# Performance work log

Measured on AMD Instinct MI355X. Metric: run time of the kernel, lower is better.

Reference implementation:

```python
import jax, jax.numpy as jnp
import numpy as np

N_NODES = 20000
N_EDGES = 160000
D_IN = 512
D_OUT = 64


def _propagate(x, src, dst, num_nodes):
    # SLPropagate with add_self_loops=False, normalize=False:
    # out[dst] += x[src]  (plain sum aggregation over incoming edges)
    return jax.ops.segment_sum(x[src], dst, num_segments=num_nodes)


def setup_inputs() -> dict:
    key = jax.random.key(0)
    k1, k2, k3, k4 = jax.random.split(key, 4)
    x = jax.random.normal(k1, (N_NODES, D_IN), dtype=jnp.float32)
    edge_index = jax.random.randint(k2, (2, N_EDGES), 0, N_NODES, dtype=jnp.int64)
    # torch.nn.Linear default init scale ~ 1/sqrt(fan_in)
    s = 1.0 / np.sqrt(D_IN)
    W1 = jax.random.uniform(k3, (D_IN, D_IN), dtype=jnp.float32, minval=-s, maxval=s)
    W2 = jax.random.uniform(k4, (D_OUT, D_IN), dtype=jnp.float32, minval=-s, maxval=s)
    return {"x": x, "edge_index": edge_index, "W1": W1, "W2": W2}


def reference(x, edge_index, W1, W2):
    num_nodes = x.shape[0]
    src, dst = edge_index[0], edge_index[1]
    h = _propagate(x, src, dst, num_nodes)          # [N, D_IN]
    h = jax.nn.relu(jnp.einsum('nd,ed->ne', h, W1))  # lin1 (no bias) + relu
    h = _propagate(h, src, dst, num_nodes)          # [N, D_IN]
    h = jnp.einsum('nd,od->no', h, W2)              # lin2 (no bias) -> [N, D_OUT]
    return jax.nn.log_softmax(h, axis=1)
```

## Files before the change

kernel.cpp:

```cpp
#include <hip/hip_runtime.h>

#define D 512
#define DOUT 64
#define MAXDEG 64

typedef __bf16 bf16x8 __attribute__((ext_vector_type(8)));
typedef float floatx4 __attribute__((ext_vector_type(4)));

__device__ __forceinline__ void async_cp16(const void* g, void* lds) {
    __builtin_amdgcn_global_load_lds(
        (__attribute__((address_space(1))) void*)(void*)g,
        (__attribute__((address_space(3))) void*)lds, 16, 0, 0);
}

__global__ __launch_bounds__(256) void prep_kernel(
        int* __restrict__ cnt, int nN, int zeroBlocks,
        __bf16* __restrict__ tzero,
        const float* __restrict__ W1, __bf16* __restrict__ w1b, int w1N8,
        const float* __restrict__ W2, __bf16* __restrict__ w2b, int w2N8) {
    int b = blockIdx.x;
    if (b < zeroBlocks) {
        int i4 = b * 1024 + threadIdx.x * 4;
        if (i4 + 3 < nN) *(int4*)(cnt + i4) = make_int4(0, 0, 0, 0);
        else {
            if (i4 + 0 < nN) cnt[i4 + 0] = 0;
            if (i4 + 1 < nN) cnt[i4 + 1] = 0;
            if (i4 + 2 < nN) cnt[i4 + 2] = 0;
        }
        return;
    }
    b -= zeroBlocks;
    if (b == 0) {
        ((unsigned*)tzero)[threadIdx.x] = 0u;
        return;
    }
    b -= 1;
    int w1Blocks = (w1N8 + 255) >> 8;
    const float* in; __bf16* outp; int n8;
    if (b < w1Blocks) { in = W1; outp = w1b; n8 = w1N8; }
    else { b -= w1Blocks; in = W2; outp = w2b; n8 = w2N8; }
    int i = b * 256 + threadIdx.x;
    if (i < n8) {
        const float4* p = (const float4*)in + (size_t)i * 2;
        float4 v0 = p[0], v1 = p[1];
        bf16x8 o;
        o[0] = (__bf16)v0.x; o[1] = (__bf16)v0.y; o[2] = (__bf16)v0.z; o[3] = (__bf16)v0.w;
        o[4] = (__bf16)v1.x; o[5] = (__bf16)v1.y; o[6] = (__bf16)v1.z; o[7] = (__bf16)v1.w;
        *((bf16x8*)outp + i) = o;
    }
}

__global__ __launch_bounds__(256, 3) void gemm1_fill(
        const float* __restrict__ Af, const __bf16* __restrict__ B,
        __bf16* __restrict__ Cout, int M, int gemmBlocks,
        const int* __restrict__ src, const int* __restrict__ dst,
        int* __restrict__ cnt, unsigned short* __restrict__ col, int nE) {
    if (blockIdx.x >= gemmBlocks) {
        int base = (blockIdx.x - gemmBlocks) * 256 + threadIdx.x;
        int stride = (gridDim.x - gemmBlocks) * 256;
        for (int e = base; e < nE; e += stride) {
            int d = dst[e];
            int slot = atomicAdd(&cnt[d], 1);
            if (slot < MAXDEG) col[(size_t)d * MAXDEG + slot] = (unsigned short)src[e];
        }
        return;
    }
    constexpr int BM = 128, BN = 128;
    __shared__ float  Asf[BM * 16 * 4];
    __shared__ __bf16 Bs[8 * BN * 8];

    const int qch = gemmBlocks >> 3, rch = gemmBlocks & 7;
    const int xcd = blockIdx.x & 7, jj = blockIdx.x >> 3;
    const int L = (xcd < rch ? xcd * (qch + 1) : rch * (qch + 1) + (xcd - rch) * qch) + jj;

    const int tid = threadIdx.x;
    const int w = tid >> 6, lane = tid & 63;
    const int wrow = w >> 1, wcol = w & 1;
    const int m0 = (L >> 2) * BM, n0 = (L & 3) * BN;
    const int quad = lane >> 4, l15 = lane & 15;

    const int srow = lane >> 3;
    const int skq  = (lane & 7) ^ (srow & 7);

    floatx4 acc[4][4] = {};

    for (int k0 = 0; k0 < D; k0 += 64) {
        #pragma unroll
        for (int c = 0; c < 8; ++c) {
            int P0 = (w * 8 + c) * 64;
            int P = P0 + lane;
            int rloc = P >> 4, cu = P & 15;
            int gr = m0 + rloc; if (gr > M - 1) gr = M - 1;
            async_cp16(Af + (size_t)gr * D + k0 + ((cu ^ (rloc & 15)) << 2),
                       &Asf[(size_t)P0 * 4]);
        }
        #pragma unroll
        for (int c = 0; c < 4; ++c) {
            int P0 = (w * 4 + c) * 64;
            int nn = n0 + (P0 >> 3) + srow;
            async_cp16(B + (size_t)nn * D + k0 + skq * 8, &Bs[(size_t)P0 * 8]);
        }
        __syncthreads();

        #pragma unroll
        for (int ksub = 0; ksub < 2; ++ksub) {
            const int kk = ksub * 4 + quad;
            bf16x8 af[4], bfr[4];
            #pragma unroll
            for (int mi = 0; mi < 4; ++mi) {
                int rr = wrow * 64 + mi * 16 + l15;
                int u0 = ((kk << 1)    ) ^ (rr & 15);
                int u1 = ((kk << 1) | 1) ^ (rr & 15);
                float4 f0 = *(const float4*)&Asf[(size_t)(rr * 16 + u0) * 4];
                float4 f1 = *(const float4*)&Asf[(size_t)(rr * 16 + u1) * 4];
                bf16x8 a_;
                a_[0] = (__bf16)f0.x; a_[1] = (__bf16)f0.y;
                a_[2] = (__bf16)f0.z; a_[3] = (__bf16)f0.w;
                a_[4] = (__bf16)f1.x; a_[5] = (__bf16)f1.y;
                a_[6] = (__bf16)f1.z; a_[7] = (__bf16)f1.w;
                af[mi] = a_;
            }
            #pragma unroll
            for (int nj = 0; nj < 4; ++nj) {
                int row = wcol * 64 + nj * 16 + l15;
                bfr[nj] = *(const bf16x8*)&Bs[(size_t)(row * 8 + (kk ^ (row & 7))) * 8];
            }
            #pragma unroll
            for (int mi = 0; mi < 4; ++mi)
                #pragma unroll
                for (int nj = 0; nj < 4; ++nj)
                    acc[mi][nj] = __builtin_amdgcn_mfma_f32_16x16x32_bf16(
                        af[mi], bfr[nj], acc[mi][nj], 0, 0, 0);
        }
        __syncthreads();
    }

    #pragma unroll
    for (int mi = 0; mi < 4; ++mi) {
        #pragma unroll
        for (int r = 0; r < 4; ++r) {
            int m = m0 + wrow * 64 + mi * 16 + quad * 4 + r;
            if (m < M) {
                #pragma unroll
                for (int nj = 0; nj < 4; ++nj) {
                    int n = n0 + wcol * 64 + nj * 16 + l15;
                    Cout[(size_t)m * D + n] = (__bf16)acc[mi][nj][r];
                }
            }
        }
    }
}

__global__ __launch_bounds__(256) void prop1_slice(
        const __bf16* __restrict__ t, const int* __restrict__ cnt,
        const unsigned short* __restrict__ col, __bf16* __restrict__ h2, int nN) {
    const int tid = threadIdx.x;
    const int w = tid >> 6, lane = tid & 63;
    const int slice = blockIdx.x & 7;
    const int grp = blockIdx.x >> 3;
    const int oct = lane & 7;
    const int n = grp * 32 + w * 8 + (lane >> 3);

    int deg = cnt[n]; if (deg > MAXDEG) deg = MAXDEG;
    int rounds = deg;
    #pragma unroll
    for (int off = 32; off >= 1; off >>= 1) {
        int o = __shfl_xor(rounds, off, 64);
        rounds = rounds > o ? rounds : o;
    }
    int rb = (rounds + 3) & ~3;

    const unsigned short* cp = col + (size_t)n * MAXDEG;
    const __bf16* tb = t + (size_t)slice * 64 + (size_t)oct * 8;

    float acc[8] = {};
    for (int r = 0; r < rb; r += 4) {
        int s0 = (r + 0 < deg) ? (int)cp[r + 0] : nN;
        int s1 = (r + 1 < deg) ? (int)cp[r + 1] : nN;
        int s2 = (r + 2 < deg) ? (int)cp[r + 2] : nN;
        int s3 = (r + 3 < deg) ? (int)cp[r + 3] : nN;
        bf16x8 v0 = *(const bf16x8*)(tb + (size_t)s0 * D);
        bf16x8 v1 = *(const bf16x8*)(tb + (size_t)s1 * D);
        bf16x8 v2 = *(const bf16x8*)(tb + (size_t)s2 * D);
        bf16x8 v3 = *(const bf16x8*)(tb + (size_t)s3 * D);
        #pragma unroll
        for (int i = 0; i < 8; ++i)
            acc[i] += ((float)v0[i] + (float)v1[i]) + ((float)v2[i] + (float)v3[i]);
    }

    bf16x8 o8;
    #pragma unroll
    for (int i = 0; i < 8; ++i) o8[i] = (__bf16)fmaxf(acc[i], 0.f);
    *(bf16x8*)(h2 + (size_t)n * D + slice * 64 + oct * 8) = o8;
}

__global__ __launch_bounds__(256) void gemm2(
        const __bf16* __restrict__ h2, const __bf16* __restrict__ B,
        __bf16* __restrict__ u, int nN) {
    __shared__ __bf16 As[16 * 512];

    const int tid = threadIdx.x;
    const int w = tid >> 6, lane = tid & 63;
    const int quad = lane >> 4, l15 = lane & 15;
    const int m0 = blockIdx.x * 16;

    #pragma unroll
    for (int c = 0; c < 4; ++c) {
        int r = w * 4 + c;
        int srcg = (lane - r) & 63;
        async_cp16(h2 + (size_t)(m0 + r) * D + srcg * 8, &As[(size_t)(r * 64) * 8]);
    }

    bf16x8 breg[16];
    #pragma unroll
    for (int kq = 0; kq < 16; ++kq)
        breg[kq] = *(const bf16x8*)(B + (size_t)(w * 16 + l15) * D + kq * 32 + quad * 8);

    __syncthreads();

    floatx4 c4 = {};
    #pragma unroll
    for (int kq = 0; kq < 16; ++kq) {
        int g = kq * 4 + quad;
        bf16x8 af = *(const bf16x8*)&As[(size_t)(l15 * 64 + ((g + l15) & 63)) * 8];
        c4 = __builtin_amdgcn_mfma_f32_16x16x32_bf16(af, breg[kq], c4, 0, 0, 0);
    }

    #pragma unroll
    for (int r = 0; r < 4; ++r) {
        int m = m0 + quad * 4 + r;
        if (m < nN)
            u[(size_t)m * DOUT + w * 16 + l15] = (__bf16)c4[r];
    }
}

__global__ __launch_bounds__(256) void prop2_lsm(const __bf16* __restrict__ u,
        const int* __restrict__ cnt, const unsigned short* __restrict__ col,
        float* __restrict__ out, int nN) {
    int n = blockIdx.x * 4 + (threadIdx.x >> 6);
    if (n >= nN) return;
    int lane = threadIdx.x & 63;
    int deg = cnt[n]; if (deg > MAXDEG) deg = MAXDEG;
    const unsigned short* cp = col + (size_t)n * MAXDEG;
    float a0 = 0.f, a1 = 0.f, a2 = 0.f, a3 = 0.f;
    float a4 = 0.f, a5 = 0.f, a6 = 0.f, a7 = 0.f;
    int e = 0;
    for (; e + 8 <= deg; e += 8) {
        int s0 = cp[e],     s1 = cp[e + 1], s2 = cp[e + 2], s3 = cp[e + 3];
        int s4 = cp[e + 4], s5 = cp[e + 5], s6 = cp[e + 6], s7 = cp[e + 7];
        a0 += (float)u[(size_t)s0 * DOUT + lane];
        a1 += (float)u[(size_t)s1 * DOUT + lane];
        a2 += (float)u[(size_t)s2 * DOUT + lane];
        a3 += (float)u[(size_t)s3 * DOUT + lane];
        a4 += (float)u[(size_t)s4 * DOUT + lane];
        a5 += (float)u[(size_t)s5 * DOUT + lane];
        a6 += (float)u[(size_t)s6 * DOUT + lane];
        a7 += (float)u[(size_t)s7 * DOUT + lane];
    }
    for (; e + 4 <= deg; e += 4) {
        int s0 = cp[e], s1 = cp[e + 1], s2 = cp[e + 2], s3 = cp[e + 3];
        a0 += (float)u[(size_t)s0 * DOUT + lane];
        a1 += (float)u[(size_t)s1 * DOUT + lane];
        a2 += (float)u[(size_t)s2 * DOUT + lane];
        a3 += (float)u[(size_t)s3 * DOUT + lane];
    }
    for (; e < deg; ++e) a0 += (float)u[(size_t)cp[e] * DOUT + lane];
    float v = ((a0 + a4) + (a1 + a5)) + ((a2 + a6) + (a3 + a7));
    float mx = v;
    #pragma unroll
    for (int off = 32; off >= 1; off >>= 1) mx = fmaxf(mx, __shfl_xor(mx, off, 64));
    float s = expf(v - mx);
    #pragma unroll
    for (int off = 32; off >= 1; off >>= 1) s += __shfl_xor(s, off, 64);
    out[(size_t)n * DOUT + lane] = v - mx - logf(s);
}


extern "C" void kernel_launch(void* const* d_in, const int* in_sizes, int n_in,
                              void* d_out, int out_size, void* d_ws, size_t ws_size,
                              hipStream_t stream) {
    const float* x  = (const float*)d_in[0];
    const int*   ei = (const int*)d_in[1];
    const float* W1 = (const float*)d_in[2];
    const float* W2 = (const float*)d_in[3];
    float* out = (float*)d_out;

    const int N = in_sizes[0] / D;
    const int E = in_sizes[1] / 2;
    const int* src = ei;
    const int* dst = ei + E;

    size_t off = 0;
    auto alloc = [&](size_t bytes) -> void* {
        void* p = (char*)d_ws + off;
        off = (off + bytes + 255) & ~(size_t)255;
        return p;
    };
    int*            cnt = (int*)alloc(sizeof(int) * (size_t)N);
    unsigned short* col = (unsigned short*)alloc(sizeof(unsigned short) * (size_t)N * MAXDEG);
    __bf16*         w1b = (__bf16*)alloc(sizeof(__bf16) * (size_t)D * D);
    __bf16*         w2b = (__bf16*)alloc(sizeof(__bf16) * (size_t)DOUT * D);
    __bf16*         t   = (__bf16*)alloc(sizeof(__bf16) * (size_t)(N + 1) * D);
    __bf16*         h2  = (__bf16*)alloc(sizeof(__bf16) * (size_t)N * D);
    __bf16*         u   = (__bf16*)alloc(sizeof(__bf16) * (size_t)N * DOUT);

    const int zeroBlocks = (N + 1023) / 1024;
    const int w1N8 = D * D / 8, w2N8 = DOUT * D / 8;
    const int cvtBlocks = (w1N8 + 255) / 256 + (w2N8 + 255) / 256;

    prep_kernel<<<zeroBlocks + 1 + cvtBlocks, 256, 0, stream>>>(
        cnt, N, zeroBlocks, t + (size_t)N * D, W1, w1b, w1N8, W2, w2b, w2N8);

    const int gemmBlocks = ((N + 127) / 128) * 4;
    gemm1_fill<<<gemmBlocks + 64, 256, 0, stream>>>(
        x, w1b, t, N, gemmBlocks, src, dst, cnt, col, E);

    prop1_slice<<<(N / 32) * 8, 256, 0, stream>>>(t, cnt, col, h2, N);

    gemm2<<<N / 16, 256, 0, stream>>>(h2, w2b, u, N);

    prop2_lsm<<<(N + 3) / 4, 256, 0, stream>>>(u, cnt, col, out, N);
}
```

Before: 156.7 us.

## Split edge fill into own kernel; stage A via registers as bf16 in LDS

The CSR fill work moves out of the fused GEMM launch into a separate one-edge-per-thread kernel. The first GEMM now loads fp32 A tiles into registers, prefetching the next k-slice while the current one computes. It converts them to bf16 once when writing LDS, so the fragment loads are direct bf16x8 reads and LDS use is halved, which allows a higher occupancy bound (4 blocks). This avoids converting each A element repeatedly inside the MFMA loop. The cost is an extra kernel launch, the fill no longer overlapping the GEMM, and more register pressure from prefetch.

```diff
diff --git a/kernel.cpp b/kernel.cpp
--- a/kernel.cpp
+++ b/kernel.cpp
@@ -50,24 +50,23 @@
     }
 }
 
-__global__ __launch_bounds__(256, 3) void gemm1_fill(
-        const float* __restrict__ Af, const __bf16* __restrict__ B,
-        __bf16* __restrict__ Cout, int M, int gemmBlocks,
+__global__ __launch_bounds__(256) void fill_kernel(
         const int* __restrict__ src, const int* __restrict__ dst,
         int* __restrict__ cnt, unsigned short* __restrict__ col, int nE) {
-    if (blockIdx.x >= gemmBlocks) {
-        int base = (blockIdx.x - gemmBlocks) * 256 + threadIdx.x;
-        int stride = (gridDim.x - gemmBlocks) * 256;
-        for (int e = base; e < nE; e += stride) {
-            int d = dst[e];
-            int slot = atomicAdd(&cnt[d], 1);
-            if (slot < MAXDEG) col[(size_t)d * MAXDEG + slot] = (unsigned short)src[e];
-        }
-        return;
-    }
+    int e = blockIdx.x * 256 + threadIdx.x;
+    if (e < nE) {
+        int d = dst[e];
+        int slot = atomicAdd(&cnt[d], 1);
+        if (slot < MAXDEG) col[(size_t)d * MAXDEG + slot] = (unsigned short)src[e];
+    }
+}
+
+__global__ __launch_bounds__(256, 4) void gemm1(
+        const float* __restrict__ Af, const __bf16* __restrict__ B,
+        __bf16* __restrict__ Cout, int M, int gemmBlocks) {
     constexpr int BM = 128, BN = 128;
-    __shared__ float  Asf[BM * 16 * 4];
-    __shared__ __bf16 Bs[8 * BN * 8];
+    __shared__ __bf16 As[BM * 8 * 8];
+    __shared__ __bf16 Bs[BN * 8 * 8];
 
     const int qch = gemmBlocks >> 3, rch = gemmBlocks & 7;
     const int xcd = blockIdx.x & 7, jj = blockIdx.x >> 3;
@@ -82,25 +81,41 @@
     const int srow = lane >> 3;
     const int skq  = (lane & 7) ^ (srow & 7);
 
+    const int arow = w * 32 + (lane >> 1);
+    const int ahalf = lane & 1;
+    int agr = m0 + arow; if (agr > M - 1) agr = M - 1;
+    const float* aptr = Af + (size_t)agr * D + ahalf * 32;
+
     floatx4 acc[4][4] = {};
-
-    for (int k0 = 0; k0 < D; k0 += 64) {
-        #pragma unroll
-        for (int c = 0; c < 8; ++c) {
-            int P0 = (w * 8 + c) * 64;
-            int P = P0 + lane;
-            int rloc = P >> 4, cu = P & 15;
-            int gr = m0 + rloc; if (gr > M - 1) gr = M - 1;
-            async_cp16(Af + (size_t)gr * D + k0 + ((cu ^ (rloc & 15)) << 2),
-                       &Asf[(size_t)P0 * 4]);
-        }
+    float4 areg[8];
+
+    #pragma unroll
+    for (int j = 0; j < 8; ++j) areg[j] = *(const float4*)(aptr + j * 4);
+
+    for (int it = 0; it < 8; ++it) {
+        const int k0 = it * 64;
         #pragma unroll
         for (int c = 0; c < 4; ++c) {
             int P0 = (w * 4 + c) * 64;
             int nn = n0 + (P0 >> 3) + srow;
             async_cp16(B + (size_t)nn * D + k0 + skq * 8, &Bs[(size_t)P0 * 8]);
         }
+        #pragma unroll
+        for (int j = 0; j < 4; ++j) {
+            int kq = ahalf * 4 + j;
+            float4 f0 = areg[2 * j], f1 = areg[2 * j + 1];
+            bf16x8 o;
+            o[0] = (__bf16)f0.x; o[1] = (__bf16)f0.y; o[2] = (__bf16)f0.z; o[3] = (__bf16)f0.w;
+            o[4] = (__bf16)f1.x; o[5] = (__bf16)f1.y; o[6] = (__bf16)f1.z; o[7] = (__bf16)f1.w;
+            *(bf16x8*)&As[(size_t)(arow * 8 + (kq ^ (arow & 7))) * 8] = o;
+        }
         __syncthreads();
+
+        if (it < 7) {
+            const float* ap = aptr + (it + 1) * 64;
+            #pragma unroll
+            for (int j = 0; j < 8; ++j) areg[j] = *(const float4*)(ap + j * 4);
+        }
 
         #pragma unroll
         for (int ksub = 0; ksub < 2; ++ksub) {
@@ -108,17 +123,8 @@
             bf16x8 af[4], bfr[4];
             #pragma unroll
             for (int mi = 0; mi < 4; ++mi) {
-                int rr = wrow * 64 + mi * 16 + l15;
-                int u0 = ((kk << 1)    ) ^ (rr & 15);
-                int u1 = ((kk << 1) | 1) ^ (rr & 15);
-                float4 f0 = *(const float4*)&Asf[(size_t)(rr * 16 + u0) * 4];
-                float4 f1 = *(const float4*)&Asf[(size_t)(rr * 16 + u1) * 4];
-                bf16x8 a_;
-                a_[0] = (__bf16)f0.x; a_[1] = (__bf16)f0.y;
-                a_[2] = (__bf16)f0.z; a_[3] = (__bf16)f0.w;
-                a_[4] = (__bf16)f1.x; a_[5] = (__bf16)f1.y;
-                a_[6] = (__bf16)f1.z; a_[7] = (__bf16)f1.w;
-                af[mi] = a_;
+                int row = wrow * 64 + mi * 16 + l15;
+                af[mi] = *(const bf16x8*)&As[(size_t)(row * 8 + (kk ^ (row & 7))) * 8];
             }
             #pragma unroll
             for (int nj = 0; nj < 4; ++nj) {
@@ -311,9 +317,10 @@
     prep_kernel<<<zeroBlocks + 1 + cvtBlocks, 256, 0, stream>>>(
         cnt, N, zeroBlocks, t + (size_t)N * D, W1, w1b, w1N8, W2, w2b, w2N8);
 
+    fill_kernel<<<(E + 255) / 256, 256, 0, stream>>>(src, dst, cnt, col, E);
+
     const int gemmBlocks = ((N + 127) / 128) * 4;
-    gemm1_fill<<<gemmBlocks + 64, 256, 0, stream>>>(
-        x, w1b, t, N, gemmBlocks, src, dst, cnt, col, E);
+    gemm1<<<gemmBlocks, 256, 0, stream>>>(x, w1b, t, N, gemmBlocks);
 
     prop1_slice<<<(N / 32) * 8, 256, 0, stream>>>(t, cnt, col, h2, N);
 
```

Result: slower. 180.2 us (+15.0%).
